# Kernel optimization log

Measured on AMD Instinct MI355X. Metric: run time of the kernel, lower is better.

Reference implementation:

```python
import jax, jax.numpy as jnp
import numpy as np


def _conv3x3(x, w):
    # x: [N,C,H,W], w: [O,I,3,3], stride 1, padding 1 -> SAME
    return jax.lax.conv_general_dilated(
        x, w, window_strides=(1, 1), padding='SAME',
        dimension_numbers=('NCHW', 'OIHW', 'NCHW'))


def setup_inputs() -> dict:
    key = jax.random.key(0)
    k1, k2, k3, k4 = jax.random.split(key, 4)
    # He-like init scale for 3x3 convs
    x = jax.random.normal(k1, (8, 1, 512, 512), dtype=jnp.float32)
    w1 = jax.random.normal(k2, (8, 1, 3, 3), dtype=jnp.float32) * (2.0 / (1 * 9)) ** 0.5
    wmid = jax.random.normal(k3, (18, 8, 8, 3, 3), dtype=jnp.float32) * (2.0 / (8 * 9)) ** 0.5
    w20 = jax.random.normal(k4, (1, 8, 3, 3), dtype=jnp.float32) * (2.0 / (8 * 9)) ** 0.5
    return {'x': x, 'w1': w1, 'wmid': wmid, 'w20': w20}


def reference(x, w1, wmid, w20):
    y = jax.nn.relu(_conv3x3(x, w1))  # conv1 + relu
    # conv2..conv19: 18 identical 8->8 conv+relu layers, scanned over stacked weights
    def body(y, w):
        return jax.nn.relu(_conv3x3(y, w)), None
    y, _ = jax.lax.scan(body, y, wmid)
    return _conv3x3(y, w20)  # conv20, no relu
```

## Files before the change

kernel.cpp:

```cpp
#include <hip/hip_runtime.h>

typedef _Float16 f16;
typedef _Float16 f16x8 __attribute__((ext_vector_type(8)));
typedef _Float16 f16x4 __attribute__((ext_vector_type(4)));
typedef float v4f __attribute__((ext_vector_type(4)));

constexpr int H = 512, W = 512, NB = 8;
constexpr int ROWS = 514;
constexpr int COLS = 528;
constexpr int CH = 8;
constexpr size_t ROWBYTES = (size_t)COLS * CH * 2;
constexpr size_t PLANE_ELEMS = (size_t)ROWS * COLS * CH;
constexpr size_t PLANE_BYTES = PLANE_ELEMS * 2;

constexpr int RSP = 145;
constexpr int RSPC = RSP * CH;
constexpr int LDS_ROWB = RSP * 16;
constexpr int WTAB_L = 3072;

__device__ __forceinline__ void gload_lds16(const void* g, void* l) {
    __builtin_amdgcn_global_load_lds(
        (const __attribute__((address_space(1))) unsigned int*)g,
        (__attribute__((address_space(3))) unsigned int*)l, 16, 0, 0);
}
__device__ __forceinline__ void gload_lds4(const void* g, void* l) {
    __builtin_amdgcn_global_load_lds(
        (const __attribute__((address_space(1))) unsigned int*)g,
        (__attribute__((address_space(3))) unsigned int*)l, 4, 0, 0);
}

__global__ void zero_borders(f16* __restrict__ base, size_t set_stride) {
    const int i = blockIdx.x * 256 + threadIdx.x;
    if (i >= 9248) return;
    const int img = blockIdx.y, set = blockIdx.z;
    int row, col;
    if (i < 1056) { row = (i < 528) ? 0 : 513; col = (i < 528) ? i : i - 528; }
    else {
        const int j = i - 1056;
        row = 1 + (j >> 4);
        const int c4 = j & 15;
        col = (c4 < 8) ? c4 : 512 + c4;
    }
    f16x8 z = {};
    f16* p = base + (size_t)set * set_stride + ((size_t)img * ROWS + row) * COLS * CH + (size_t)col * CH;
    *(f16x8*)p = z;
}

__global__ void build_wtab(const float* __restrict__ wmid,
                           const float* __restrict__ w20,
                           f16* __restrict__ wtab) {
    const int l = blockIdx.x;
    const int lane = threadIdx.x;
    const float* wt = (l < 18) ? wmid + (size_t)l * 576 : w20;
    const int COUT = (l < 18) ? 8 : 1;
    const int n = lane & 15, q = lane >> 4;
#pragma unroll
    for (int g = 0; g < 3; ++g) {
        const int t = g * 4 + q;
        f16x8 hv, lv;
#pragma unroll
        for (int j = 0; j < 8; ++j) {
            float wv = 0.f;
            if (n < 8) {
                if (t <= 8 && n < COUT) wv = wt[(n * 8 + j) * 9 + t];
            } else {
                const int o = n - 8;
                if (t >= 3 && o < COUT) wv = wt[(o * 8 + j) * 9 + (t - 3)];
            }
            const f16 h = (f16)wv;
            hv[j] = h;
            lv[j] = (f16)(wv - (float)h);
        }
        f16* dst = wtab + (size_t)l * WTAB_L + (g * 2) * 512 + lane * 8;
        *(f16x8*)dst = hv;
        *(f16x8*)(dst + 512) = lv;
    }
}

__global__ __launch_bounds__(256) void conv1_kernel(
    const float* __restrict__ in, const float* __restrict__ wt,
    f16* __restrict__ out)
{
    const int x0 = (blockIdx.x * 64 + threadIdx.x) * 4;
    const int y  = blockIdx.y * 4 + threadIdx.y;
    const int b  = blockIdx.z;
    const float* inb = in + (size_t)b * H * W;

    float patch[3][6];
#pragma unroll
    for (int r = 0; r < 3; ++r) {
        const int iy = y - 1 + r;
        if (iy >= 0 && iy < H) {
            const float* rp = inb + (size_t)iy * W;
            const float4 v = *(const float4*)(rp + x0);
            patch[r][1] = v.x; patch[r][2] = v.y; patch[r][3] = v.z; patch[r][4] = v.w;
            patch[r][0] = (x0 > 0)     ? rp[x0 - 1] : 0.f;
            patch[r][5] = (x0 + 4 < W) ? rp[x0 + 4] : 0.f;
        } else {
#pragma unroll
            for (int k = 0; k < 6; ++k) patch[r][k] = 0.f;
        }
    }

    float acc[8][4];
#pragma unroll
    for (int o = 0; o < 8; ++o) {
        const float* wo = wt + o * 9;
        float a0 = 0.f, a1 = 0.f, a2 = 0.f, a3 = 0.f;
#pragma unroll
        for (int r = 0; r < 3; ++r)
#pragma unroll
            for (int k = 0; k < 3; ++k) {
                const float wv = wo[r * 3 + k];
                a0 = fmaf(wv, patch[r][k + 0], a0);
                a1 = fmaf(wv, patch[r][k + 1], a1);
                a2 = fmaf(wv, patch[r][k + 2], a2);
                a3 = fmaf(wv, patch[r][k + 3], a3);
            }
        acc[o][0] = a0; acc[o][1] = a1; acc[o][2] = a2; acc[o][3] = a3;
    }

#pragma unroll
    for (int j = 0; j < 4; ++j) {
        f16x8 hv;
#pragma unroll
        for (int o = 0; o < 8; ++o)
            hv[o] = (f16)fmaxf(acc[o][j], 0.f);
        const size_t off = (((size_t)b * ROWS + (y + 1)) * COLS + (x0 + j + 8)) * CH;
        *(f16x8*)(out + off) = hv;
    }
}

__global__ __launch_bounds__(256) void conv2fused(
    const f16* __restrict__ in,
    const f16* __restrict__ wtA, const f16* __restrict__ wtB,
    f16* __restrict__ outp)
{
    __shared__ __align__(16) f16 aring[10 * RSPC];
    __shared__ __align__(16) f16 inring[12 * RSPC];

    const int wave = threadIdx.x >> 6, lane = threadIdx.x & 63;
    const int img = blockIdx.x, xt = blockIdx.y;
    const int x0 = xt * 128;
    const int base = blockIdx.z * 32;

    f16x8 ahiW[3], aloW[3], bhiW[3], bloW[3];
#pragma unroll
    for (int g = 0; g < 3; ++g) {
        const f16* wa = wtA + (g * 2) * 512 + lane * 8;
        ahiW[g] = *(const f16x8*)wa;  aloW[g] = *(const f16x8*)(wa + 512);
        const f16* wb = wtB + (g * 2) * 512 + lane * 8;
        bhiW[g] = *(const f16x8*)wb;  bloW[g] = *(const f16x8*)(wb + 512);
    }

    const char* src = (const char*)in + (size_t)img * PLANE_BYTES + (size_t)x0 * 16;

    auto stage = [&](int r0, int cnt) {
        for (int qq = wave; qq < cnt * 3; qq += 4) {
            const int rr = qq / 3, c = qq % 3;
            const int row = r0 + rr;
            const int rowc = min(max(row, 0), 513);
            const int slot = ((row % 12) + 12) % 12;
            const char* gs = src + (size_t)rowc * ROWBYTES;
            char* ld = (char*)inring + slot * LDS_ROWB;
            if (c < 2) gload_lds16(gs + c * 1024 + lane * 16, ld + c * 1024);
            else       gload_lds4(gs + 2048 + lane * 4, ld + 2048);
        }
    };

    const int n = lane & 15, q = lane >> 4;
    int tyv[3], txv[3];
#pragma unroll
    for (int g = 0; g < 3; ++g) { const int t = g * 4 + q; tyv[g] = t / 3 - 1; txv[g] = t % 3 - 1; }
    const int rowoff = q >> 1, choff = (q & 1) * 4;
    const bool xe0 = (xt == 0), xe3 = (xt == 3);

    auto computeA = [&](int rA) {
        int irow[3];
#pragma unroll
        for (int g = 0; g < 3; ++g) irow[g] = ((rA + tyv[g] + 12) % 12) * RSPC;
        const int gyA = rA + rowoff;
        const int wrow = (gyA % 10) * RSPC;
        const bool zr = (gyA == 0) || (gyA == 513);
#pragma unroll
        for (int s = 0; s < 9; ++s) {
            v4f acc = {0.f,0.f,0.f,0.f}, acc2 = {0.f,0.f,0.f,0.f};
#pragma unroll
            for (int g = 0; g < 3; ++g) {
                const f16x8 xv = *(const f16x8*)&inring[irow[g] + (16 * s + n + txv[g]) * CH];
                acc  = __builtin_amdgcn_mfma_f32_16x16x32_f16(ahiW[g], xv, acc,  0, 0, 0);
                acc2 = __builtin_amdgcn_mfma_f32_16x16x32_f16(aloW[g], xv, acc2, 0, 0, 0);
            }
            const v4f res = acc + acc2;
            f16x4 hv;
#pragma unroll
            for (int c = 0; c < 4; ++c) hv[c] = (f16)fmaxf(res[c], 0.f);
            if (zr || (xe0 && s == 0 && n == 7) || (xe3 && s == 8 && n == 8)) {
                hv[0] = (f16)0.f; hv[1] = (f16)0.f; hv[2] = (f16)0.f; hv[3] = (f16)0.f;
            }
            *(f16x4*)&aring[wrow + (16 * s + n) * CH + choff] = hv;
        }
    };

    auto computeB = [&](int rB) {
        int brow[3];
#pragma unroll
        for (int g = 0; g < 3; ++g) brow[g] = ((rB + tyv[g]) % 10) * RSPC;
        const int gyB = rB + rowoff;
        f16* orow = outp + ((size_t)img * ROWS + gyB) * COLS * CH + (size_t)(x0 + 8) * CH + choff;
#pragma unroll
        for (int s = 0; s < 8; ++s) {
            v4f acc = {0.f,0.f,0.f,0.f}, acc2 = {0.f,0.f,0.f,0.f};
#pragma unroll
            for (int g = 0; g < 3; ++g) {
                const f16x8 xv = *(const f16x8*)&aring[brow[g] + (16 * s + n + txv[g] + 8) * CH];
                acc  = __builtin_amdgcn_mfma_f32_16x16x32_f16(bhiW[g], xv, acc,  0, 0, 0);
                acc2 = __builtin_amdgcn_mfma_f32_16x16x32_f16(bloW[g], xv, acc2, 0, 0, 0);
            }
            const v4f res = acc + acc2;
            f16x4 hv;
#pragma unroll
            for (int c = 0; c < 4; ++c) hv[c] = (f16)fmaxf(res[c], 0.f);
            *(f16x4*)(orow + (size_t)(16 * s + n) * CH) = hv;
        }
    };

    stage(base - 1, 12);
    __syncthreads();
    if (wave == 0) computeA(base);

    for (int t = 0; t < 4; ++t) {
        computeA(base + 8 * t + 2 + 2 * wave);
        __syncthreads();
        if (t < 3) stage(base + 8 * t + 11, 8);
        computeB(base + 8 * t + 1 + 2 * wave);
        __syncthreads();
    }
}

template<bool RELU, bool FINAL>
__global__ __launch_bounds__(256) void convmfma(
    const f16* __restrict__ in, const f16* __restrict__ wtab_l,
    f16* __restrict__ outp, float* __restrict__ out_final)
{
    __shared__ __align__(16) f16 lds[2][10 * RSPC];

    const int wave = threadIdx.x >> 6, lane = threadIdx.x & 63;
    const int img = blockIdx.x;
    const int x0 = blockIdx.y * 128;
    const int ybase = blockIdx.z * 32;

    f16x8 bhi[3], blo[3];
#pragma unroll
    for (int g = 0; g < 3; ++g) {
        const f16* wp = wtab_l + (g * 2) * 512 + lane * 8;
        bhi[g] = *(const f16x8*)wp;
        blo[g] = *(const f16x8*)(wp + 512);
    }

    const char* src = (const char*)in + (size_t)img * PLANE_BYTES + (size_t)x0 * 16;
    auto stage = [&](int buf, int y0) {
        char* dst = (char*)&lds[buf][0];
        for (int qq = wave; qq < 30; qq += 4) {
            const int r = qq / 3, c = qq % 3;
            const char* gs = src + (size_t)(y0 + r) * ROWBYTES;
            char* ld = dst + r * LDS_ROWB;
            if (c < 2) gload_lds16(gs + c * 1024 + lane * 16, ld + c * 1024);
            else       gload_lds4(gs + 2048 + lane * 4, ld + 2048);
        }
    };

    const int n = lane & 15, q = lane >> 4, m = lane & 15;
    int abase[3];
#pragma unroll
    for (int g = 0; g < 3; ++g) {
        const int t = g * 4 + q;
        const int ty = t / 3 - 1, tx = t % 3 - 1;
        abase[g] = (2 * wave + ty + 1) * RSP + (m + tx + 8);
    }
    const int rowoff = q >> 1;
    const int choff = (q & 1) * 4;

    stage(0, ybase);
    __syncthreads();

    for (int t = 0; t < 4; ++t) {
        if (t < 3) stage((t + 1) & 1, ybase + 8 * (t + 1));
        const f16* L = &lds[t & 1][0];
        const int Y = ybase + 8 * t + 2 * wave;
#pragma unroll
        for (int s = 0; s < 8; ++s) {
            v4f acc = {0.f,0.f,0.f,0.f}, acc2 = {0.f,0.f,0.f,0.f};
#pragma unroll
            for (int g = 0; g < 3; ++g) {
                const f16x8 xv = *(const f16x8*)&L[(abase[g] + 16 * s) * CH];
                acc  = __builtin_amdgcn_mfma_f32_16x16x32_f16(bhi[g], xv, acc,  0, 0, 0);
                acc2 = __builtin_amdgcn_mfma_f32_16x16x32_f16(blo[g], xv, acc2, 0, 0, 0);
            }
            const v4f res = acc + acc2;
            if constexpr (!FINAL) {
                f16x4 hv;
#pragma unroll
                for (int c = 0; c < 4; ++c) {
                    float v = res[c];
                    if (RELU) v = fmaxf(v, 0.f);
                    hv[c] = (f16)v;
                }
                const int gy = Y + rowoff + 1;
                const int gx = x0 + 16 * s + n + 8;
                *(f16x4*)(outp + ((size_t)img * ROWS + gy) * COLS * CH + (size_t)gx * CH + choff) = hv;
            } else {
                if ((q & 1) == 0) {
                    const int gy = Y + rowoff, gx = x0 + 16 * s + n;
                    out_final[((size_t)img * H + gy) * W + gx] = res[0];
                }
            }
        }
        if (t < 3) __syncthreads();
    }
}

extern "C" void kernel_launch(void* const* d_in, const int* in_sizes, int n_in,
                              void* d_out, int out_size, void* d_ws, size_t ws_size,
                              hipStream_t stream) {
    const float* x    = (const float*)d_in[0];
    const float* w1   = (const float*)d_in[1];
    const float* wmid = (const float*)d_in[2];
    const float* w20  = (const float*)d_in[3];
    float* out = (float*)d_out;

    const size_t wtab_bytes = (size_t)19 * WTAB_L * 2;
    int g = NB;
    while (g > 1 && 2 * (size_t)g * PLANE_BYTES + wtab_bytes > ws_size) g >>= 1;

    f16* act0 = (f16*)d_ws;
    f16* act1 = act0 + (size_t)g * PLANE_ELEMS;
    f16* wtab = act1 + (size_t)g * PLANE_ELEMS;

    zero_borders<<<dim3(37, g, 2), 256, 0, stream>>>(act0, (size_t)g * PLANE_ELEMS);
    build_wtab<<<19, 64, 0, stream>>>(wmid, w20, wtab);

    for (int b0 = 0; b0 < NB; b0 += g) {
        conv1_kernel<<<dim3(2, 128, g), dim3(64, 4), 0, stream>>>(
            x + (size_t)b0 * H * W, w1, act0);
        for (int k = 0; k < 9; ++k) {
            const f16* s0 = (k & 1) ? act1 : act0;
            f16*       d0 = (k & 1) ? act0 : act1;
            conv2fused<<<dim3(g, 4, 16), 256, 0, stream>>>(
                s0, wtab + (size_t)(2 * k) * WTAB_L, wtab + (size_t)(2 * k + 1) * WTAB_L, d0);
        }
        convmfma<false, true><<<dim3(g, 4, 16), 256, 0, stream>>>(
            act1, wtab + (size_t)18 * WTAB_L, nullptr, out + (size_t)b0 * H * W);
    }
}
```

Before: 317.3 us.

## Retile fused conv pair to 64x64 tiles with deeper ring and single sync per step

The fused two-layer conv kernel now works on 64-column by 64-row tiles instead of 128x32, with larger LDS rings (21 input rows, 18 intermediate rows). The staging of the next rows, the first conv and the second conv now run in the same loop step with one barrier per step instead of two, so loads and compute overlap more. Narrower tiles reduce halo recompute along y but add more halo columns relative to the tile width, and the grid changes to 8x8 tiles per image.

```diff
diff --git a/kernel.cpp b/kernel.cpp
--- a/kernel.cpp
+++ b/kernel.cpp
@@ -17,6 +17,12 @@
 constexpr int RSPC = RSP * CH;
 constexpr int LDS_ROWB = RSP * 16;
 constexpr int WTAB_L = 3072;
+
+constexpr int FRSP = 81;
+constexpr int FRSPC = FRSP * CH;
+constexpr int FROWB = FRSP * 16;
+constexpr int INR = 21;
+constexpr int ARR = 18;
 
 __device__ __forceinline__ void gload_lds16(const void* g, void* l) {
     __builtin_amdgcn_global_load_lds(
@@ -136,13 +142,13 @@
     const f16* __restrict__ wtA, const f16* __restrict__ wtB,
     f16* __restrict__ outp)
 {
-    __shared__ __align__(16) f16 aring[10 * RSPC];
-    __shared__ __align__(16) f16 inring[12 * RSPC];
+    __shared__ __align__(16) f16 aring[ARR * FRSPC];
+    __shared__ __align__(16) f16 inring[INR * FRSPC];
 
     const int wave = threadIdx.x >> 6, lane = threadIdx.x & 63;
     const int img = blockIdx.x, xt = blockIdx.y;
-    const int x0 = xt * 128;
-    const int base = blockIdx.z * 32;
+    const int x0 = xt * 64;
+    const int base = blockIdx.z * 64;
 
     f16x8 ahiW[3], aloW[3], bhiW[3], bloW[3];
 #pragma unroll
@@ -156,15 +162,14 @@
     const char* src = (const char*)in + (size_t)img * PLANE_BYTES + (size_t)x0 * 16;
 
     auto stage = [&](int r0, int cnt) {
-        for (int qq = wave; qq < cnt * 3; qq += 4) {
-            const int rr = qq / 3, c = qq % 3;
+        for (int rr = wave; rr < cnt; rr += 4) {
             const int row = r0 + rr;
             const int rowc = min(max(row, 0), 513);
-            const int slot = ((row % 12) + 12) % 12;
+            const int slot = ((row % INR) + INR) % INR;
             const char* gs = src + (size_t)rowc * ROWBYTES;
-            char* ld = (char*)inring + slot * LDS_ROWB;
-            if (c < 2) gload_lds16(gs + c * 1024 + lane * 16, ld + c * 1024);
-            else       gload_lds4(gs + 2048 + lane * 4, ld + 2048);
+            char* ld = (char*)inring + slot * FROWB;
+            gload_lds16(gs + lane * 16, ld);
+            if (lane < 16) gload_lds16(gs + 1024 + lane * 16, ld + 1024);
         }
     };
 
@@ -173,17 +178,20 @@
 #pragma unroll
     for (int g = 0; g < 3; ++g) { const int t = g * 4 + q; tyv[g] = t / 3 - 1; txv[g] = t % 3 - 1; }
     const int rowoff = q >> 1, choff = (q & 1) * 4;
-    const bool xe0 = (xt == 0), xe3 = (xt == 3);
+    const bool xe0 = (xt == 0), xe7 = (xt == 7);
 
     auto computeA = [&](int rA) {
         int irow[3];
 #pragma unroll
-        for (int g = 0; g < 3; ++g) irow[g] = ((rA + tyv[g] + 12) % 12) * RSPC;
+        for (int g = 0; g < 3; ++g) {
+            const int r = rA + tyv[g];
+            irow[g] = (((r % INR) + INR) % INR) * FRSPC;
+        }
         const int gyA = rA + rowoff;
-        const int wrow = (gyA % 10) * RSPC;
+        const int wrow = (gyA % ARR) * FRSPC;
         const bool zr = (gyA == 0) || (gyA == 513);
 #pragma unroll
-        for (int s = 0; s < 9; ++s) {
+        for (int s = 0; s < 5; ++s) {
             v4f acc = {0.f,0.f,0.f,0.f}, acc2 = {0.f,0.f,0.f,0.f};
 #pragma unroll
             for (int g = 0; g < 3; ++g) {
@@ -195,7 +203,7 @@
             f16x4 hv;
 #pragma unroll
             for (int c = 0; c < 4; ++c) hv[c] = (f16)fmaxf(res[c], 0.f);
-            if (zr || (xe0 && s == 0 && n == 7) || (xe3 && s == 8 && n == 8)) {
+            if (zr || (xe0 && s == 0 && n == 7) || (xe7 && s == 4 && n == 8)) {
                 hv[0] = (f16)0.f; hv[1] = (f16)0.f; hv[2] = (f16)0.f; hv[3] = (f16)0.f;
             }
             *(f16x4*)&aring[wrow + (16 * s + n) * CH + choff] = hv;
@@ -205,11 +213,11 @@
     auto computeB = [&](int rB) {
         int brow[3];
 #pragma unroll
-        for (int g = 0; g < 3; ++g) brow[g] = ((rB + tyv[g]) % 10) * RSPC;
+        for (int g = 0; g < 3; ++g) brow[g] = ((rB + tyv[g]) % ARR) * FRSPC;
         const int gyB = rB + rowoff;
         f16* orow = outp + ((size_t)img * ROWS + gyB) * COLS * CH + (size_t)(x0 + 8) * CH + choff;
 #pragma unroll
-        for (int s = 0; s < 8; ++s) {
+        for (int s = 0; s < 4; ++s) {
             v4f acc = {0.f,0.f,0.f,0.f}, acc2 = {0.f,0.f,0.f,0.f};
 #pragma unroll
             for (int g = 0; g < 3; ++g) {
@@ -225,14 +233,14 @@
         }
     };
 
-    stage(base - 1, 12);
+    stage(base - 1, 21);
     __syncthreads();
-    if (wave == 0) computeA(base);
-
-    for (int t = 0; t < 4; ++t) {
-        computeA(base + 8 * t + 2 + 2 * wave);
-        __syncthreads();
-        if (t < 3) stage(base + 8 * t + 11, 8);
+    for (int p = wave; p < 5; p += 4) computeA(base + 2 * p);
+    __syncthreads();
+
+    for (int t = 0; t < 8; ++t) {
+        if (t < 6) stage(base + 8 * t + 20, 8);
+        if (t < 7) computeA(base + 8 * t + 10 + 2 * wave);
         computeB(base + 8 * t + 1 + 2 * wave);
         __syncthreads();
     }
@@ -346,7 +354,7 @@
         for (int k = 0; k < 9; ++k) {
             const f16* s0 = (k & 1) ? act1 : act0;
             f16*       d0 = (k & 1) ? act0 : act1;
-            conv2fused<<<dim3(g, 4, 16), 256, 0, stream>>>(
+            conv2fused<<<dim3(g, 8, 8), 256, 0, stream>>>(
                 s0, wtab + (size_t)(2 * k) * WTAB_L, wtab + (size_t)(2 * k + 1) * WTAB_L, d0);
         }
         convmfma<false, true><<<dim3(g, 4, 16), 256, 0, stream>>>(
```

After: 332.9 us. 4.9% more time.
